# Kernel tuning notes

Hardware: AMD Instinct MI355X
Metric: run time of the kernel (lower is better)

The kernel has to match this reference:

```python
import jax, jax.numpy as jnp
import numpy as np

CH = 128
GROUPS = 8
EPS = 1e-5

def group_norm(x, w, b):
    B, C, H, W = x.shape
    g = x.reshape(B, GROUPS, C // GROUPS, H, W)
    mean = g.mean(axis=(2, 3, 4), keepdims=True)
    var = g.var(axis=(2, 3, 4), keepdims=True)
    g = (g - mean) * jax.lax.rsqrt(var + EPS)
    g = g.reshape(B, C, H, W)
    return g * w[None, :, None, None] + b[None, :, None, None]

def setup_inputs() -> dict:
    key = jax.random.key(0)
    ks = jax.random.split(key, 7)
    C = CH
    x = jax.random.normal(ks[0], (8, C, 64, 64), dtype=jnp.float32)
    gn_w = jnp.ones((C,), dtype=jnp.float32)
    gn_b = jnp.zeros((C,), dtype=jnp.float32)
    s = 1.0 / np.sqrt(C)
    qkv_w = jax.random.normal(ks[1], (3 * C, C), dtype=jnp.float32) * s
    qkv_b = jax.random.normal(ks[2], (3 * C,), dtype=jnp.float32) * 0.01
    proj_w = jax.random.normal(ks[3], (C, C), dtype=jnp.float32) * s
    proj_b = jax.random.normal(ks[4], (C,), dtype=jnp.float32) * 0.01
    return {"x": x, "gn_w": gn_w, "gn_b": gn_b, "qkv_w": qkv_w,
            "qkv_b": qkv_b, "proj_w": proj_w, "proj_b": proj_b}

def reference(x, gn_w, gn_b, qkv_w, qkv_b, proj_w, proj_b):
    B, C, H, W = x.shape
    h = group_norm(x, gn_w, gn_b)
    # 1x1 conv == per-pixel matmul over channels
    qkv = jnp.einsum('bchw,oc->bohw', h, qkv_w) + qkv_b[None, :, None, None]
    q, k, v = jnp.split(qkv.reshape(B, 3 * C, H * W), 3, axis=1)  # each [B,C,N]
    scale = C ** (-0.5)
    attn = jax.nn.softmax(jnp.einsum('bci,bcj->bij', q * scale, k), axis=-1)
    out = jnp.einsum('bij,bcj->bci', attn, v).reshape(B, C, H, W)
    out = jnp.einsum('bchw,oc->bohw', out, proj_w) + proj_b[None, :, None, None]
    return x + out
```

## Files before the change

### kernel.cpp

```cpp
#include <hip/hip_runtime.h>
#include <stdint.h>


typedef __attribute__((ext_vector_type(8))) short short8;
typedef __attribute__((ext_vector_type(4))) float f32x4;
typedef __attribute__((ext_vector_type(16))) float f32x16;

#define MFMA_BF16(a, b, c) __builtin_amdgcn_mfma_f32_16x16x32_bf16((a), (b), (c), 0, 0, 0)
#define MFMA32(a, b, c) __builtin_amdgcn_mfma_f32_32x32x16_bf16((a), (b), (c), 0, 0, 0)
#define EXP2(x) __builtin_amdgcn_exp2f(x)

#define QSCALE 0.12751743f

__device__ __forceinline__ unsigned short f2bf(float f) {
    unsigned int u = __builtin_bit_cast(unsigned int, f);
    u += 0x7FFFu + ((u >> 16) & 1u);
    return (unsigned short)(u >> 16);
}
__device__ __forceinline__ float bf2f(unsigned int lo16) {
    return __builtin_bit_cast(float, lo16 << 16);
}
__device__ __forceinline__ short8 ldg8(const unsigned short* p) {
    return __builtin_bit_cast(short8, *(const uint4*)p);
}
__device__ __forceinline__ unsigned int cvtpk(float lo, float hi) {
    unsigned int r;
    asm("v_cvt_pk_bf16_f32 %0, %1, %2" : "=v"(r) : "v"(lo), "v"(hi));
    return r;
}
__device__ __forceinline__ void gload16(const void* g, void* l) {
    __builtin_amdgcn_global_load_lds(
        (__attribute__((address_space(1))) void*)g,
        (__attribute__((address_space(3))) void*)l, 16, 0, 0);
}

__global__ __launch_bounds__(256) void k_pre(const float* __restrict__ x,
                                             float* __restrict__ sums,
                                             const float* __restrict__ qkv_w,
                                             const float* __restrict__ proj_w,
                                             unsigned short* __restrict__ wq,
                                             unsigned short* __restrict__ wp) {
    if (blockIdx.x >= 1024) {
        int i = ((blockIdx.x - 1024) * 256 + threadIdx.x) * 4;
        const float* src; unsigned short* dst; int off;
        if (i < 49152) { src = qkv_w; dst = wq; off = i; }
        else           { src = proj_w; dst = wp; off = i - 49152; }
        float4 v = *(const float4*)(src + off);
        uint2 pk;
        pk.x = (unsigned int)f2bf(v.x) | ((unsigned int)f2bf(v.y) << 16);
        pk.y = (unsigned int)f2bf(v.z) | ((unsigned int)f2bf(v.w) << 16);
        *(uint2*)(dst + off) = pk;
        return;
    }
    int g     = blockIdx.x >> 4;
    int slice = blockIdx.x & 15;
    const float* p = x + (size_t)g * 65536 + slice * 4096;
    float s = 0.f, sq = 0.f;
#pragma unroll
    for (int i = 0; i < 4; ++i) {
        float4 v = *(const float4*)(p + threadIdx.x * 4 + i * 1024);
        s  += v.x + v.y + v.z + v.w;
        sq += v.x*v.x + v.y*v.y + v.z*v.z + v.w*v.w;
    }
#pragma unroll
    for (int m = 1; m < 64; m <<= 1) { s += __shfl_xor(s, m, 64); sq += __shfl_xor(sq, m, 64); }
    __shared__ float ss[4], ssq[4];
    int w = threadIdx.x >> 6;
    if ((threadIdx.x & 63) == 0) { ss[w] = s; ssq[w] = sq; }
    __syncthreads();
    if (threadIdx.x == 0) {
        atomicAdd(&sums[g * 2],     ss[0] + ss[1] + ss[2] + ss[3]);
        atomicAdd(&sums[g * 2 + 1], ssq[0] + ssq[1] + ssq[2] + ssq[3]);
    }
}

__global__ __launch_bounds__(256) void k_qkv(const float* __restrict__ x,
                                             const float* __restrict__ sums,
                                             const float* __restrict__ gn_w,
                                             const float* __restrict__ gn_b,
                                             const unsigned short* __restrict__ wq,
                                             const float* __restrict__ qkv_b,
                                             unsigned short* __restrict__ q_ws,
                                             unsigned short* __restrict__ k_ws,
                                             unsigned short* __restrict__ v_ws) {
    __shared__ unsigned short h_lds[64][136];
    const int tid  = threadIdx.x;
    const int b    = blockIdx.x >> 6;
    const int n0   = (blockIdx.x & 63) << 6;
    const int lane = tid & 63, wave = tid >> 6;
    const int l15  = lane & 15, q4 = lane >> 4;

    {
        int cb = tid >> 4;
        int nn = (tid & 15) << 2;
#pragma unroll
        for (int k = 0; k < 8; ++k) {
            int c = cb + (k << 4);
            float4 v = *(const float4*)(x + ((size_t)(b * 128 + c) << 12) + n0 + nn);
            int g = c >> 4;
            float ts = sums[(b * 8 + g) * 2];
            float tq = sums[(b * 8 + g) * 2 + 1];
            float mean = ts * (1.f / 65536.f);
            float var  = tq * (1.f / 65536.f) - mean * mean;
            float rstd = rsqrtf(var + 1e-5f);
            float ga = gn_w[c] * rstd;
            float be = gn_b[c] - mean * ga;
            h_lds[nn + 0][c] = f2bf(v.x * ga + be);
            h_lds[nn + 1][c] = f2bf(v.y * ga + be);
            h_lds[nn + 2][c] = f2bf(v.z * ga + be);
            h_lds[nn + 3][c] = f2bf(v.w * ga + be);
        }
    }
    __syncthreads();

    short8 bfrag[4][4];
#pragma unroll
    for (int nt = 0; nt < 4; ++nt)
#pragma unroll
        for (int ks = 0; ks < 4; ++ks)
            bfrag[nt][ks] = *(const short8*)&h_lds[nt * 16 + l15][ks * 32 + q4 * 8];

#pragma unroll
    for (int ot = 0; ot < 6; ++ot) {
        int o0 = wave * 96 + ot * 16;
        short8 af[4];
#pragma unroll
        for (int ks = 0; ks < 4; ++ks)
            af[ks] = ldg8(wq + (size_t)(o0 + l15) * 128 + ks * 32 + q4 * 8);

        if (o0 < 256) {
            float bias[4];
#pragma unroll
            for (int r = 0; r < 4; ++r) bias[r] = qkv_b[o0 + q4 * 4 + r];
            float qs = (o0 < 128) ? QSCALE : 1.0f;
#pragma unroll
            for (int nt = 0; nt < 4; ++nt) {
                f32x4 acc = {0.f, 0.f, 0.f, 0.f};
#pragma unroll
                for (int ks = 0; ks < 4; ++ks)
                    acc = MFMA_BF16(af[ks], bfrag[nt][ks], acc);
                int n = n0 + nt * 16 + l15;
                unsigned short* dst = (o0 < 128) ? q_ws : k_ws;
                int oo = (o0 < 128) ? o0 : (o0 - 128);
                unsigned int lo = (unsigned int)f2bf((acc[0] + bias[0]) * qs) |
                                  ((unsigned int)f2bf((acc[1] + bias[1]) * qs) << 16);
                unsigned int hi = (unsigned int)f2bf((acc[2] + bias[2]) * qs) |
                                  ((unsigned int)f2bf((acc[3] + bias[3]) * qs) << 16);
                uint2 pk; pk.x = lo; pk.y = hi;
                *(uint2*)&dst[((size_t)(b * 4096 + n) << 7) + oo + q4 * 4] = pk;
            }
        } else {
            int c = o0 - 256 + l15;
            float vb = qkv_b[o0 + l15];
            unsigned short* vrow = v_ws + ((size_t)(b * 128 + c) << 12) + n0;
#pragma unroll
            for (int nt = 0; nt < 4; ++nt) {
                f32x4 acc = {0.f, 0.f, 0.f, 0.f};
#pragma unroll
                for (int ks = 0; ks < 4; ++ks)
                    acc = MFMA_BF16(bfrag[nt][ks], af[ks], acc);
                unsigned int lo = (unsigned int)f2bf(acc[0] + vb) |
                                  ((unsigned int)f2bf(acc[1] + vb) << 16);
                unsigned int hi = (unsigned int)f2bf(acc[2] + vb) |
                                  ((unsigned int)f2bf(acc[3] + vb) << 16);
                uint2 pk; pk.x = lo; pk.y = hi;
                *(uint2*)&vrow[nt * 16 + q4 * 4] = pk;
            }
        }
    }
}

__global__ __launch_bounds__(512, 2) void k_attn_part(const unsigned short* __restrict__ q_ws,
                                                      const unsigned short* __restrict__ k_ws,
                                                      const unsigned short* __restrict__ v_ws,
                                                      unsigned short* __restrict__ o_part,
                                                      float* __restrict__ ml) {
    __shared__ unsigned short K0[64][128];
    __shared__ unsigned short K1[64][128];
    __shared__ unsigned short V0[128][64];
    __shared__ unsigned short V1[128][64];
    __shared__ unsigned short P_lds[128][64];

    const int tid   = threadIdx.x;
    const int chunk = blockIdx.x & 3;
    const int tile  = (blockIdx.x >> 2) & 31;
    const int b     = blockIdx.x >> 7;
    const int i0    = tile << 7;
    const int lane  = tid & 63, wave = tid >> 6;
    const int ih    = wave >> 1, jh = wave & 1;
    const int l31   = lane & 31, h = lane >> 5;

    short8 qf[8];
    {
        const unsigned short* qp =
            q_ws + ((size_t)(b * 4096 + i0 + ih * 32 + l31) << 7) + h * 8;
#pragma unroll
        for (int ks = 0; ks < 8; ++ks) qf[ks] = ldg8(qp + ks * 16);
    }

    f32x16 acc[2];
#pragma unroll
    for (int e = 0; e < 16; ++e) { acc[0][e] = 0.f; acc[1][e] = 0.f; }
    float l_run = 0.f;

    const unsigned short* kbase = k_ws + ((size_t)b << 19) + ((size_t)chunk << 17);
    int ksrc[2];
#pragma unroll
    for (int q = 0; q < 2; ++q) {
        int c   = q * 512 + tid;
        int row = c >> 4;
        ksrc[q] = row * 16 + ((c & 15) ^ (row & 15));
    }
    const unsigned short* vlane = v_ws + ((size_t)b << 19) +
        ((size_t)(tid >> 3) << 12) + (chunk << 10) +
        ((((tid & 7) ^ ((tid >> 3) & 7) ^ wave)) << 3);

#define STAGE(T, KD, VD)                                                              \
  do {                                                                                \
    _Pragma("unroll")                                                                 \
    for (int q = 0; q < 2; ++q)                                                       \
      gload16(kbase + (size_t)(T) * 8192 + ksrc[q] * 8,                               \
              (char*)(&KD[0][0]) + q * 8192 + wave * 1024);                           \
    _Pragma("unroll")                                                                 \
    for (int q = 0; q < 2; ++q)                                                       \
      gload16(vlane + (size_t)q * 262144 + (T) * 64,                                  \
              (char*)(&VD[0][0]) + q * 8192 + wave * 1024);                           \
  } while (0)

#define BAR_A()                                                                       \
  do {                                                                                \
    asm volatile("s_waitcnt vmcnt(0)" ::: "memory");                                  \
    __builtin_amdgcn_s_barrier();                                                     \
    __builtin_amdgcn_sched_barrier(0);                                                \
  } while (0)
#define BAR_B()                                                                       \
  do {                                                                                \
    asm volatile("s_waitcnt lgkmcnt(0)" ::: "memory");                                \
    __builtin_amdgcn_s_barrier();                                                     \
    __builtin_amdgcn_sched_barrier(0);                                                \
  } while (0)

    const int krow = jh * 32 + l31;
    const int ksw  = l31 & 15;
    const int vk   = (l31 & 7) ^ (l31 >> 3);
    const int irow = ih * 32 + l31;
    const int pkey = (irow ^ (irow >> 3)) & 7;

    STAGE(0, K0, V0);

#define ATTN_ITER(IT, KR, VR, KP, VP)                                                 \
  do {                                                                                \
    BAR_A();                 \
    if ((IT) < 15) STAGE((IT) + 1, KP, VP);               \
    f32x16 s;        \
    _Pragma("unroll")                                                                 \
    for (int e = 0; e < 16; ++e) s[e] = 0.f;                                          \
    _Pragma("unroll")                                                                 \
    for (int ks = 0; ks < 8; ++ks) {                                                  \
      short8 kf = *(const short8*)&KR[krow][((ks * 2 + h) ^ ksw) << 3];               \
      s = MFMA32(kf, qf[ks], s);                                                      \
    }                                                                                 \
    float pv[16];                                        \
    _Pragma("unroll")                                                                 \
    for (int e = 0; e < 16; ++e) pv[e] = EXP2(fminf(s[e], 30.f));                     \
    l_run += (((pv[0] + pv[1]) + (pv[2] + pv[3])) +                                   \
              ((pv[4] + pv[5]) + (pv[6] + pv[7]))) +                                  \
             (((pv[8] + pv[9]) + (pv[10] + pv[11])) +                                 \
              ((pv[12] + pv[13]) + (pv[14] + pv[15])));                               \
    {                                                                                 \
      char* prow = (char*)&P_lds[irow][0];                                            \
      _Pragma("unroll")                                                               \
      for (int rr = 0; rr < 4; ++rr) {                                                \
        uint2 pk;                                                                     \
        pk.x = cvtpk(pv[rr * 4 + 0], pv[rr * 4 + 1]);                                 \
        pk.y = cvtpk(pv[rr * 4 + 2], pv[rr * 4 + 3]);                                 \
        *(uint2*)(prow + ((((jh << 2) + rr) ^ pkey) << 4) + (h << 3)) = pk;           \
      }                                                                               \
    }                                                                                 \
    BAR_B();                                     \
    _Pragma("unroll")                                                                 \
    for (int ks = 0; ks < 4; ++ks) {                                                  \
      short8 pf = *(const short8*)((const char*)&P_lds[irow][0] +                     \
                                   (((ks * 2 + h) ^ pkey) << 4));                     \
      _Pragma("unroll")                                                               \
      for (int ct = 0; ct < 2; ++ct) {                                                \
        short8 vf = *(const short8*)&VR[jh * 64 + ct * 32 + l31]                      \
                        [((ks * 2 + h) ^ vk ^ (ct << 2)) << 3];                       \
        acc[ct] = MFMA32(pf, vf, acc[ct]);                                            \
      }                                                                               \
    }                                                                                 \
  } while (0)

    for (int ib = 0; ib < 8; ++ib) {
        ATTN_ITER(ib * 2,     K0, V0, K1, V1);
        ATTN_ITER(ib * 2 + 1, K1, V1, K0, V0);
    }
#undef ATTN_ITER
#undef STAGE
#undef BAR_A
#undef BAR_B

    __syncthreads();
    float* Lp = (float*)(&K0[0][0]);
    float l2 = l_run + __shfl_xor(l_run, 32);
    if (h == 0) Lp[jh * 128 + irow] = l2;
    __syncthreads();

    float rl[16];
#pragma unroll
    for (int r = 0; r < 16; ++r) {
        int il = (r & 3) + ((r >> 2) << 3) + (h << 2);
        rl[r] = 1.0f / (Lp[ih * 32 + il] + Lp[128 + ih * 32 + il]);
    }
#pragma unroll
    for (int ct = 0; ct < 2; ++ct)
#pragma unroll
        for (int r = 0; r < 16; ++r) {
            int row = ih * 32 + (r & 3) + ((r >> 2) << 3) + (h << 2);
            o_part[(((size_t)(b * 4096 + i0 + row) * 4 + chunk) << 7) +
                   jh * 64 + ct * 32 + l31] = f2bf(acc[ct][r] * rl[r]);
        }
    if (tid < 128) {
        ml[(b * 4096 + i0 + tid) * 4 + chunk] = __log2f(Lp[tid] + Lp[128 + tid]);
    }
}

__global__ __launch_bounds__(256) void k_merge_proj(const unsigned short* __restrict__ o_part,
                                                    const float* __restrict__ ml,
                                                    const float* __restrict__ x,
                                                    const unsigned short* __restrict__ wp,
                                                    const float* __restrict__ proj_b,
                                                    float* __restrict__ out) {
    __shared__ unsigned short O_lds[64][136];
    __shared__ float wgt[64][4];
    const int tid  = threadIdx.x;
    const int b    = blockIdx.x >> 6;
    const int tile = blockIdx.x & 63;
    const int i0   = tile << 6;
    const int lane = tid & 63, wave = tid >> 6;
    const int l15  = lane & 15, q4 = lane >> 4;

    if (tid < 64) {
        size_t mb = (size_t)(b * 4096 + i0 + tid) * 4;
        float m0 = ml[mb + 0], m1 = ml[mb + 1], m2 = ml[mb + 2], m3 = ml[mb + 3];
        float M = fmaxf(fmaxf(m0, m1), fmaxf(m2, m3));
        float w0 = EXP2(m0 - M), w1 = EXP2(m1 - M), w2 = EXP2(m2 - M), w3 = EXP2(m3 - M);
        float rW = 1.0f / (w0 + w1 + w2 + w3);
        wgt[tid][0] = w0 * rW; wgt[tid][1] = w1 * rW;
        wgt[tid][2] = w2 * rW; wgt[tid][3] = w3 * rW;
    }
    __syncthreads();

    {
        int n = tid >> 2, q = tid & 3;
        float w[4];
#pragma unroll
        for (int ch = 0; ch < 4; ++ch) w[ch] = wgt[n][ch];
        size_t rbase = ((size_t)(b * 4096 + i0 + n) * 4) << 7;
#pragma unroll
        for (int g = 0; g < 4; ++g) {
            float acc[8];
#pragma unroll
            for (int e = 0; e < 8; ++e) acc[e] = 0.f;
#pragma unroll
            for (int ch = 0; ch < 4; ++ch) {
                const unsigned short* p = o_part + rbase + (ch << 7) + q * 32 + g * 8;
                uint4 v = *(const uint4*)p;
                float wc = w[ch];
                acc[0] += wc * bf2f(v.x & 0xFFFF); acc[1] += wc * bf2f(v.x >> 16);
                acc[2] += wc * bf2f(v.y & 0xFFFF); acc[3] += wc * bf2f(v.y >> 16);
                acc[4] += wc * bf2f(v.z & 0xFFFF); acc[5] += wc * bf2f(v.z >> 16);
                acc[6] += wc * bf2f(v.w & 0xFFFF); acc[7] += wc * bf2f(v.w >> 16);
            }
            uint4 pk;
            pk.x = (unsigned int)f2bf(acc[0]) | ((unsigned int)f2bf(acc[1]) << 16);
            pk.y = (unsigned int)f2bf(acc[2]) | ((unsigned int)f2bf(acc[3]) << 16);
            pk.z = (unsigned int)f2bf(acc[4]) | ((unsigned int)f2bf(acc[5]) << 16);
            pk.w = (unsigned int)f2bf(acc[6]) | ((unsigned int)f2bf(acc[7]) << 16);
            *(uint4*)&O_lds[n][q * 32 + g * 8] = pk;
        }
    }
    __syncthreads();

    short8 bfrag[4][4];
#pragma unroll
    for (int nt = 0; nt < 4; ++nt)
#pragma unroll
        for (int ks = 0; ks < 4; ++ks)
            bfrag[nt][ks] = *(const short8*)&O_lds[nt * 16 + l15][ks * 32 + q4 * 8];

#pragma unroll
    for (int ot = 0; ot < 2; ++ot) {
        int o0 = wave * 32 + ot * 16;
        short8 af[4];
#pragma unroll
        for (int ks = 0; ks < 4; ++ks)
            af[ks] = ldg8(wp + (size_t)(o0 + l15) * 128 + ks * 32 + q4 * 8);
        float pb[4];
#pragma unroll
        for (int r = 0; r < 4; ++r) pb[r] = proj_b[o0 + q4 * 4 + r];

#pragma unroll
        for (int nt = 0; nt < 4; ++nt) {
            f32x4 acc = {0.f, 0.f, 0.f, 0.f};
#pragma unroll
            for (int ks = 0; ks < 4; ++ks)
                acc = MFMA_BF16(af[ks], bfrag[nt][ks], acc);
#pragma unroll
            for (int r = 0; r < 4; ++r) {
                size_t idx = ((size_t)(b * 128 + o0 + q4 * 4 + r) << 12) + i0 + nt * 16 + l15;
                out[idx] = x[idx] + acc[r] + pb[r];
            }
        }
    }
}

extern "C" void kernel_launch(void* const* d_in, const int* in_sizes, int n_in,
                              void* d_out, int out_size, void* d_ws, size_t ws_size,
                              hipStream_t stream) {
    const float* x      = (const float*)d_in[0];
    const float* gn_w   = (const float*)d_in[1];
    const float* gn_b   = (const float*)d_in[2];
    const float* qkv_w  = (const float*)d_in[3];
    const float* qkv_b  = (const float*)d_in[4];
    const float* proj_w = (const float*)d_in[5];
    const float* proj_b = (const float*)d_in[6];
    float* out = (float*)d_out;

    char* ws = (char*)d_ws;
    float* sums           = (float*)ws;
    unsigned short* wq    = (unsigned short*)(ws + 4096);
    unsigned short* wp    = (unsigned short*)(ws + 4096 + 98304);
    unsigned short* q_ws  = (unsigned short*)(ws + ((size_t)1  << 20));
    unsigned short* k_ws  = (unsigned short*)(ws + ((size_t)9  << 20));
    unsigned short* v_ws  = (unsigned short*)(ws + ((size_t)17 << 20));
    unsigned short* o_part= (unsigned short*)(ws + ((size_t)25 << 20));
    float* ml             = (float*)(ws + ((size_t)57 << 20));

    hipMemsetAsync(sums, 0, 512, stream);
    k_pre<<<1088, 256, 0, stream>>>(x, sums, qkv_w, proj_w, wq, wp);
    k_qkv<<<512, 256, 0, stream>>>(x, sums, gn_w, gn_b, wq, qkv_b, q_ws, k_ws, v_ws);
    k_attn_part<<<1024, 512, 0, stream>>>(q_ws, k_ws, v_ws, o_part, ml);
    k_merge_proj<<<512, 256, 0, stream>>>(o_part, ml, x, wp, proj_b, out);
}
```

Measured before the change: 198.4 us.

## Keep softmax probabilities in registers via permlane swap, split PV over keys

The P tile no longer goes through LDS and the second barrier per iteration is gone. Each wave repacks its exp'd scores into MFMA A-operand layout with permlane32_swap. It then multiplies against its own 32 keys for all 128 value channels, which doubles the accumulators to four 32x32 tiles. The two jh halves' partial outputs are reduced through LDS once in the epilogue. This cuts per-iteration LDS traffic and barrier stalls, at the cost of more accumulator registers, which could hurt occupancy at 2 blocks per CU.

```diff
diff --git a/kernel.cpp b/kernel.cpp
--- a/kernel.cpp
+++ b/kernel.cpp
@@ -179,7 +179,7 @@
     __shared__ unsigned short K1[64][128];
     __shared__ unsigned short V0[128][64];
     __shared__ unsigned short V1[128][64];
-    __shared__ unsigned short P_lds[128][64];
+    __shared__ float Lp[256];
 
     const int tid   = threadIdx.x;
     const int chunk = blockIdx.x & 3;
@@ -198,9 +198,11 @@
         for (int ks = 0; ks < 8; ++ks) qf[ks] = ldg8(qp + ks * 16);
     }
 
-    f32x16 acc[2];
-#pragma unroll
-    for (int e = 0; e < 16; ++e) { acc[0][e] = 0.f; acc[1][e] = 0.f; }
+    f32x16 acc[4];
+#pragma unroll
+    for (int ct = 0; ct < 4; ++ct)
+#pragma unroll
+        for (int e = 0; e < 16; ++e) acc[ct][e] = 0.f;
     float l_run = 0.f;
 
     const unsigned short* kbase = k_ws + ((size_t)b << 19) + ((size_t)chunk << 17);
@@ -233,25 +235,18 @@
     __builtin_amdgcn_s_barrier();                                                     \
     __builtin_amdgcn_sched_barrier(0);                                                \
   } while (0)
-#define BAR_B()                                                                       \
-  do {                                                                                \
-    asm volatile("s_waitcnt lgkmcnt(0)" ::: "memory");                                \
-    __builtin_amdgcn_s_barrier();                                                     \
-    __builtin_amdgcn_sched_barrier(0);                                                \
-  } while (0)
 
     const int krow = jh * 32 + l31;
     const int ksw  = l31 & 15;
     const int vk   = (l31 & 7) ^ (l31 >> 3);
     const int irow = ih * 32 + l31;
-    const int pkey = (irow ^ (irow >> 3)) & 7;
 
     STAGE(0, K0, V0);
 
 #define ATTN_ITER(IT, KR, VR, KP, VP)                                                 \
   do {                                                                                \
-    BAR_A();                 \
-    if ((IT) < 15) STAGE((IT) + 1, KP, VP);               \
+    BAR_A();                      \
+    if ((IT) < 15) STAGE((IT) + 1, KP, VP);           \
     f32x16 s;        \
     _Pragma("unroll")                                                                 \
     for (int e = 0; e < 16; ++e) s[e] = 0.f;                                          \
@@ -260,35 +255,34 @@
       short8 kf = *(const short8*)&KR[krow][((ks * 2 + h) ^ ksw) << 3];               \
       s = MFMA32(kf, qf[ks], s);                                                      \
     }                                                                                 \
-    float pv[16];                                        \
-    _Pragma("unroll")                                                                 \
-    for (int e = 0; e < 16; ++e) pv[e] = EXP2(fminf(s[e], 30.f));                     \
-    l_run += (((pv[0] + pv[1]) + (pv[2] + pv[3])) +                                   \
-              ((pv[4] + pv[5]) + (pv[6] + pv[7]))) +                                  \
-             (((pv[8] + pv[9]) + (pv[10] + pv[11])) +                                 \
-              ((pv[12] + pv[13]) + (pv[14] + pv[15])));                               \
-    {                                                                                 \
-      char* prow = (char*)&P_lds[irow][0];                                            \
+    float pvv[16];                         \
+    _Pragma("unroll")                                                                 \
+    for (int e = 0; e < 16; ++e) pvv[e] = EXP2(fminf(s[e], 30.f));                    \
+    l_run += (((pvv[0] + pvv[1]) + (pvv[2] + pvv[3])) +                               \
+              ((pvv[4] + pvv[5]) + (pvv[6] + pvv[7]))) +                              \
+             (((pvv[8] + pvv[9]) + (pvv[10] + pvv[11])) +                             \
+              ((pvv[12] + pvv[13]) + (pvv[14] + pvv[15])));                           \
+    short8 paf[2];     \
+    _Pragma("unroll")                                                                 \
+    for (int ks = 0; ks < 2; ++ks) {                                                  \
+      const float* pp = pvv + ks * 8;                                                 \
+      unsigned int Wa = cvtpk(pp[0], pp[1]);      \
+      unsigned int Wc = cvtpk(pp[2], pp[3]);               \
+      unsigned int Wb = cvtpk(pp[4], pp[5]);               \
+      unsigned int Wd = cvtpk(pp[6], pp[7]);               \
+      auto r1 = __builtin_amdgcn_permlane32_swap(Wa, Wb, false, false);               \
+      auto r2 = __builtin_amdgcn_permlane32_swap(Wc, Wd, false, false);               \
+      uint4 aw; aw.x = r1[0]; aw.y = r2[0]; aw.z = r1[1]; aw.w = r2[1];               \
+      paf[ks] = __builtin_bit_cast(short8, aw);                  \
+    }                                                                                 \
+    _Pragma("unroll")                                                                 \
+    for (int ks = 0; ks < 2; ++ks)                                                    \
       _Pragma("unroll")                                                               \
-      for (int rr = 0; rr < 4; ++rr) {                                                \
-        uint2 pk;                                                                     \
-        pk.x = cvtpk(pv[rr * 4 + 0], pv[rr * 4 + 1]);                                 \
-        pk.y = cvtpk(pv[rr * 4 + 2], pv[rr * 4 + 3]);                                 \
-        *(uint2*)(prow + ((((jh << 2) + rr) ^ pkey) << 4) + (h << 3)) = pk;           \
+      for (int ct = 0; ct < 4; ++ct) {                                                \
+        short8 vf = *(const short8*)&VR[ct * 32 + l31]                                \
+            [((jh * 4 + ks * 2 + h) ^ vk ^ ((ct & 1) << 2)) << 3];                    \
+        acc[ct] = MFMA32(paf[ks], vf, acc[ct]);                                       \
       }                                                                               \
-    }                                                                                 \
-    BAR_B();                                     \
-    _Pragma("unroll")                                                                 \
-    for (int ks = 0; ks < 4; ++ks) {                                                  \
-      short8 pf = *(const short8*)((const char*)&P_lds[irow][0] +                     \
-                                   (((ks * 2 + h) ^ pkey) << 4));                     \
-      _Pragma("unroll")                                                               \
-      for (int ct = 0; ct < 2; ++ct) {                                                \
-        short8 vf = *(const short8*)&VR[jh * 64 + ct * 32 + l31]                      \
-                        [((ks * 2 + h) ^ vk ^ (ct << 2)) << 3];                       \
-        acc[ct] = MFMA32(pf, vf, acc[ct]);                                            \
-      }                                                                               \
-    }                                                                                 \
   } while (0)
 
     for (int ib = 0; ib < 8; ++ib) {
@@ -298,28 +292,64 @@
 #undef ATTN_ITER
 #undef STAGE
 #undef BAR_A
-#undef BAR_B
-
-    __syncthreads();
-    float* Lp = (float*)(&K0[0][0]);
+
+    __syncthreads();
     float l2 = l_run + __shfl_xor(l_run, 32);
     if (h == 0) Lp[jh * 128 + irow] = l2;
-    __syncthreads();
-
-    float rl[16];
-#pragma unroll
-    for (int r = 0; r < 16; ++r) {
-        int il = (r & 3) + ((r >> 2) << 3) + (h << 2);
-        rl[r] = 1.0f / (Lp[ih * 32 + il] + Lp[128 + ih * 32 + il]);
-    }
-#pragma unroll
-    for (int ct = 0; ct < 2; ++ct)
+    float* ObLow  = (ih < 2) ? (float*)&K0[0][0] : (float*)&K1[0][0];
+    float* ObHigh = (ih < 2) ? (float*)&V0[0][0] : (float*)&V1[0][0];
+    const int vbase = (ih & 1) * 32;
+    if (jh) {
+#pragma unroll
+        for (int cc = 0; cc < 2; ++cc)
+#pragma unroll
+            for (int r = 0; r < 16; ++r) {
+                int il = (r & 3) + ((r >> 2) << 3) + (h << 2);
+                ObLow[(vbase + il) * 64 + cc * 32 + l31] = (cc == 0) ? acc[0][r] : acc[1][r];
+            }
+    } else {
+#pragma unroll
+        for (int cc = 0; cc < 2; ++cc)
+#pragma unroll
+            for (int r = 0; r < 16; ++r) {
+                int il = (r & 3) + ((r >> 2) << 3) + (h << 2);
+                ObHigh[(vbase + il) * 64 + cc * 32 + l31] = (cc == 0) ? acc[2][r] : acc[3][r];
+            }
+    }
+    __syncthreads();
+    {
+        float rl[16];
 #pragma unroll
         for (int r = 0; r < 16; ++r) {
-            int row = ih * 32 + (r & 3) + ((r >> 2) << 3) + (h << 2);
-            o_part[(((size_t)(b * 4096 + i0 + row) * 4 + chunk) << 7) +
-                   jh * 64 + ct * 32 + l31] = f2bf(acc[ct][r] * rl[r]);
-        }
+            int il = (r & 3) + ((r >> 2) << 3) + (h << 2);
+            rl[r] = 1.0f / (Lp[ih * 32 + il] + Lp[128 + ih * 32 + il]);
+        }
+        if (jh) {
+#pragma unroll
+            for (int cc = 0; cc < 2; ++cc)
+#pragma unroll
+                for (int r = 0; r < 16; ++r) {
+                    int il = (r & 3) + ((r >> 2) << 3) + (h << 2);
+                    float own = (cc == 0) ? acc[2][r] : acc[3][r];
+                    float v = own + ObHigh[(vbase + il) * 64 + cc * 32 + l31];
+                    int row = ih * 32 + il;
+                    o_part[(((size_t)(b * 4096 + i0 + row) * 4 + chunk) << 7) +
+                           64 + cc * 32 + l31] = f2bf(v * rl[r]);
+                }
+        } else {
+#pragma unroll
+            for (int cc = 0; cc < 2; ++cc)
+#pragma unroll
+                for (int r = 0; r < 16; ++r) {
+                    int il = (r & 3) + ((r >> 2) << 3) + (h << 2);
+                    float own = (cc == 0) ? acc[0][r] : acc[1][r];
+                    float v = own + ObLow[(vbase + il) * 64 + cc * 32 + l31];
+                    int row = ih * 32 + il;
+                    o_part[(((size_t)(b * 4096 + i0 + row) * 4 + chunk) << 7) +
+                           cc * 32 + l31] = f2bf(v * rl[r]);
+                }
+        }
+    }
     if (tid < 128) {
         ml[(b * 4096 + i0 + tid) * 4 + chunk] = __log2f(Lp[tid] + Lp[128 + tid]);
     }
```

Result: no change. 200.6 us (+1.1%).
